# Kernel tuning notes

Hardware: AMD Instinct MI355X
Metric: run time of the kernel (lower is better)

The kernel has to match this reference:

```python
import jax, jax.numpy as jnp
import numpy as np

N, E, F_IN, C, H = 50000, 800000, 256, 128, 2
NEG_SLOPE = 0.2


def setup_inputs() -> dict:
    key = jax.random.key(0)
    ks = jax.random.split(key, 8)
    x = jax.random.normal(ks[0], (N, F_IN), dtype=jnp.float32)
    edge_index = jax.random.randint(ks[1], (2, E), 0, N, dtype=jnp.int64)
    # GATConv params (PyG: lin weight [H*C, F_IN], att_src/att_dst [H, C], bias [H*C])
    s_lin = 1.0 / np.sqrt(F_IN)
    W = jax.random.uniform(ks[2], (H * C, F_IN), minval=-s_lin, maxval=s_lin, dtype=jnp.float32)
    att_src = jax.random.normal(ks[3], (H, C), dtype=jnp.float32) * 0.1
    att_dst = jax.random.normal(ks[4], (H, C), dtype=jnp.float32) * 0.1
    bias = jnp.zeros((H * C,), dtype=jnp.float32)
    # trailing nn.Linear(H*C, C)
    s_l = 1.0 / np.sqrt(H * C)
    lin_w = jax.random.uniform(ks[5], (C, H * C), minval=-s_l, maxval=s_l, dtype=jnp.float32)
    lin_b = jax.random.uniform(ks[6], (C,), minval=-s_l, maxval=s_l, dtype=jnp.float32)
    return {"x": x, "edge_index": edge_index, "W": W, "att_src": att_src,
            "att_dst": att_dst, "bias": bias, "lin_w": lin_w, "lin_b": lin_b}


def _gat_forward(x, edge_index, W, att_src, att_dst, bias, lin_w, lin_b):
    # add self-loops (PyG default add_self_loops=True)
    loop = jnp.arange(N, dtype=edge_index.dtype)
    src = jnp.concatenate([edge_index[0], loop])  # [E+N]
    dst = jnp.concatenate([edge_index[1], loop])  # [E+N]

    h = (x @ W.T).reshape(N, H, C)                # [N, H, C]
    a_src = jnp.einsum('nhc,hc->nh', h, att_src)  # [N, H]
    a_dst = jnp.einsum('nhc,hc->nh', h, att_dst)  # [N, H]

    e = a_src[src] + a_dst[dst]                   # [E+N, H]
    e = jnp.where(e > 0, e, NEG_SLOPE * e)        # LeakyReLU(0.2)

    # softmax over edges grouped by destination node
    m = jax.ops.segment_max(e, dst, num_segments=N)          # [N, H]
    m = jnp.where(jnp.isfinite(m), m, 0.0)
    ex = jnp.exp(e - jax.lax.stop_gradient(m)[dst])
    denom = jax.ops.segment_sum(ex, dst, num_segments=N)     # [N, H]
    alpha = ex / jnp.maximum(denom[dst], 1e-16)               # [E+N, H]

    msg = h[src] * alpha[:, :, None]                          # [E+N, H, C]
    out = jax.ops.segment_sum(msg, dst, num_segments=N)       # [N, H, C]
    out = out.reshape(N, H * C) + bias

    out = jax.nn.elu(out)
    return out @ lin_w.T + lin_b                               # [N, C]


def reference(x, edge_index, W, att_src, att_dst, bias, lin_w, lin_b):
    return _gat_forward(x, edge_index, W, att_src, att_dst, bias, lin_w, lin_b)
```

## Files before the change

kernel.cpp:

```cpp
#include <hip/hip_runtime.h>
#include <hip/hip_fp16.h>
#include <math.h>

#define NN 50000
#define EE 800000
#define ET (EE + NN)
#define FIN 256
#define CCOUT 128
#define HH 2
#define HC 256
#define NEG 0.2f
#define RCAP 64

#define NB_XPREP (NN / 4)

#define PREP_W_BLOCKS 64
#define PREP_LW_BLOCKS 32
#define PREP_GRID (3 + PREP_W_BLOCKS + PREP_LW_BLOCKS)

#define G1X 391
#define G1Y 2
#define NB_G1 (G1X * G1Y)
#define NB_SCAT4 ((ET + 1023) / 1024)
#define PAIR_HEAD (2 * NB_G1)
#define NB_FUSE2 (NB_SCAT4 + NB_G1)

typedef __attribute__((ext_vector_type(8))) short short8;
typedef __attribute__((ext_vector_type(4))) float floatx4;
typedef _Float16 half2v __attribute__((ext_vector_type(2)));

__device__ __forceinline__ unsigned short f2bf(float f)
{
    union { float f; unsigned int u; } x; x.f = f;
    unsigned int r = x.u + 0x7fffu + ((x.u >> 16) & 1u);
    return (unsigned short)(r >> 16);
}
__device__ __forceinline__ unsigned short f2h(float f)
{
    __half h = __float2half_rn(f);
    return *(const unsigned short*)&h;
}
__device__ __forceinline__ unsigned int permb(unsigned int a, unsigned int b, unsigned int s)
{
    return __builtin_amdgcn_perm(a, b, s);
}
__device__ __forceinline__ float fdot2u(unsigned int a, unsigned int b, float c)
{
    union { unsigned int u; half2v h; } x, y;
    x.u = a; y.u = b;
    return __builtin_amdgcn_fdot2(x.h, y.h, c, false);
}

__device__ __forceinline__ int load_idx(const int* ei32, int is64, int pos)
{
    return is64 ? ei32[2 * pos] : ei32[pos];
}

__global__ __launch_bounds__(256) void prep_kernel(const float* __restrict__ W,
                                                   const float* __restrict__ att_s,
                                                   const float* __restrict__ att_d,
                                                   const float* __restrict__ lin_w,
                                                   const int* __restrict__ ei32,
                                                   float* __restrict__ was,
                                                   float* __restrict__ wad,
                                                   unsigned short* __restrict__ Wb,
                                                   unsigned short* __restrict__ linwb,
                                                   int* __restrict__ flag)
{
    int b = blockIdx.x, t = threadIdx.x;
    if (b == 0) {
        if (t < 64) {
            int v = ei32[2 * t + 1];
            unsigned long long m = __ballot(v != 0);
            if (t == 0) *flag = (m == 0ull) ? 1 : 0;
        }
    } else if (b <= 2) {
        int hd = b - 1;
        float as = 0.f, ad = 0.f;
        for (int c = 0; c < CCOUT; c++) {
            float wv = W[(size_t)(hd * CCOUT + c) * FIN + t];
            as += att_s[hd * CCOUT + c] * wv;
            ad += att_d[hd * CCOUT + c] * wv;
        }
        was[hd * FIN + t] = as;
        wad[hd * FIN + t] = ad;
    } else if (b < 3 + PREP_W_BLOCKS) {
        int i = (b - 3) * 256 + t;
        float4 v = *(const float4*)(W + (size_t)i * 4);
        ushort4 o;
        o.x = f2bf(v.x); o.y = f2bf(v.y); o.z = f2bf(v.z); o.w = f2bf(v.w);
        *(ushort4*)(Wb + (size_t)i * 4) = o;
    } else {
        int i = (b - 3 - PREP_W_BLOCKS) * 256 + t;
        float4 v = *(const float4*)(lin_w + (size_t)i * 4);
        ushort4 o;
        o.x = f2bf(v.x); o.y = f2bf(v.y); o.z = f2bf(v.z); o.w = f2bf(v.w);
        *(ushort4*)(linwb + (size_t)i * 4) = o;
    }
}

__global__ __launch_bounds__(256) void xprep_kernel(const float* __restrict__ x,
                                                    const float* __restrict__ was,
                                                    const float* __restrict__ wad,
                                                    unsigned short* __restrict__ xb,
                                                    float* __restrict__ a_s,
                                                    float* __restrict__ a_d)
{
    int b = blockIdx.x, t = threadIdx.x;
    int w = t >> 6, l = t & 63;
    int n = b * 4 + w;
    float4 xv = *(const float4*)(x + (size_t)n * FIN + l * 4);
    ushort4 xs;
    xs.x = f2bf(xv.x); xs.y = f2bf(xv.y); xs.z = f2bf(xv.z); xs.w = f2bf(xv.w);
    *(ushort4*)(xb + (size_t)n * FIN + l * 4) = xs;

    float4 s0 = *(const float4*)(was + l * 4);
    float4 s1 = *(const float4*)(was + FIN + l * 4);
    float4 d0 = *(const float4*)(wad + l * 4);
    float4 d1 = *(const float4*)(wad + FIN + l * 4);
    float vs0 = xv.x * s0.x + xv.y * s0.y + xv.z * s0.z + xv.w * s0.w;
    float vs1 = xv.x * s1.x + xv.y * s1.y + xv.z * s1.z + xv.w * s1.w;
    float vd0 = xv.x * d0.x + xv.y * d0.y + xv.z * d0.z + xv.w * d0.w;
    float vd1 = xv.x * d1.x + xv.y * d1.y + xv.z * d1.z + xv.w * d1.w;
#pragma unroll
    for (int off = 32; off > 0; off >>= 1) {
        vs0 += __shfl_down(vs0, off);
        vs1 += __shfl_down(vs1, off);
        vd0 += __shfl_down(vd0, off);
        vd1 += __shfl_down(vd1, off);
    }
    if (l == 0) {
        a_s[n * 2 + 0] = vs0; a_s[n * 2 + 1] = vs1;
        a_d[n * 2 + 0] = vd0; a_d[n * 2 + 1] = vd1;
    }
}

template <bool ADD_BIAS, bool OUT_BF16>
__global__ __launch_bounds__(256) void gemm_mfma(const unsigned short* __restrict__ A,
                                                 const unsigned short* __restrict__ B,
                                                 const float* __restrict__ bias,
                                                 void* __restrict__ Cout,
                                                 int M, int N, int K)
{
    const int LDT = 40;
    __shared__ unsigned short As[128 * LDT];
    __shared__ unsigned short Bs[128 * LDT];

    int tid = threadIdx.x;
    int wave = tid >> 6, lane = tid & 63;
    int wr = wave >> 1, wc = wave & 1;
    int quad = lane >> 4, l16 = lane & 15;
    int bm0 = blockIdx.x * 128;
    int bn0 = blockIdx.y * 128;

    floatx4 acc[4][4] = {};

    for (int kk = 0; kk < K; kk += 32) {
#pragma unroll
        for (int p = 0; p < 2; p++) {
            int idx = p * 256 + tid;
            int row = idx >> 2, seg = idx & 3;
            int grow = bm0 + row; if (grow >= M) grow = M - 1;
            uint4 va = *(const uint4*)(A + (size_t)grow * K + kk + seg * 8);
            *(uint4*)(&As[row * LDT + seg * 8]) = va;
            uint4 vb = *(const uint4*)(B + (size_t)(bn0 + row) * K + kk + seg * 8);
            *(uint4*)(&Bs[row * LDT + seg * 8]) = vb;
        }
        __syncthreads();

        short8 af[4], bfr[4];
#pragma unroll
        for (int mi = 0; mi < 4; mi++)
            af[mi] = *(const short8*)(&As[(wr * 64 + mi * 16 + l16) * LDT + quad * 8]);
#pragma unroll
        for (int ni = 0; ni < 4; ni++)
            bfr[ni] = *(const short8*)(&Bs[(wc * 64 + ni * 16 + l16) * LDT + quad * 8]);
#pragma unroll
        for (int mi = 0; mi < 4; mi++)
#pragma unroll
            for (int ni = 0; ni < 4; ni++)
                acc[mi][ni] = __builtin_amdgcn_mfma_f32_16x16x32_bf16(af[mi], bfr[ni], acc[mi][ni], 0, 0, 0);
        __syncthreads();
    }

#pragma unroll
    for (int mi = 0; mi < 4; mi++) {
#pragma unroll
        for (int ni = 0; ni < 4; ni++) {
            int col = bn0 + wc * 64 + ni * 16 + l16;
#pragma unroll
            for (int r = 0; r < 4; r++) {
                int row = bm0 + wr * 64 + mi * 16 + quad * 4 + r;
                if (row < M) {
                    float v = acc[mi][ni][r];
                    if (ADD_BIAS) v += bias[col];
                    if (OUT_BF16)
                        ((unsigned short*)Cout)[(size_t)row * N + col] = f2bf(v);
                    else
                        ((float*)Cout)[(size_t)row * N + col] = v;
                }
            }
        }
    }
}

__global__ __launch_bounds__(256) void scatter_gemm1_kernel(
        const int* __restrict__ ei32, const int* __restrict__ flag,
        int* __restrict__ cnt,
        const float* __restrict__ a_s, const float* __restrict__ a_d,
        uint2* __restrict__ rec,
        const unsigned short* __restrict__ A,
        const unsigned short* __restrict__ B,
        unsigned short* __restrict__ hb)
{
    const int LDT = 40;
    __shared__ unsigned short As[128 * LDT];
    __shared__ unsigned short Bs[128 * LDT];

    int b = blockIdx.x, tid = threadIdx.x;
    int sb = -1, gb = -1;
    if (b < PAIR_HEAD) {
        if (b & 1) sb = b >> 1; else gb = b >> 1;
    } else {
        sb = NB_G1 + (b - PAIR_HEAD);
    }

    if (sb >= 0) {
        int base = sb * 1024 + tid;
        int is64 = *flag;
        int ss[4], dd[4];
#pragma unroll
        for (int k = 0; k < 4; k++) {
            int e = base + k * 256;
            ss[k] = -1; dd[k] = 0;
            if (e < ET) {
                if (e < EE) { ss[k] = load_idx(ei32, is64, e); dd[k] = load_idx(ei32, is64, EE + e); }
                else { ss[k] = dd[k] = e - EE; }
            }
        }
        int rk[4];
#pragma unroll
        for (int k = 0; k < 4; k++)
            rk[k] = (ss[k] >= 0) ? atomicAdd(&cnt[dd[k] << 4], 1) : 0;
#pragma unroll
        for (int k = 0; k < 4; k++) {
            if (ss[k] < 0) continue;
            float e0 = a_s[ss[k] * 2 + 0] + a_d[dd[k] * 2 + 0];
            float e1 = a_s[ss[k] * 2 + 1] + a_d[dd[k] * 2 + 1];
            e0 = e0 > 0.f ? e0 : NEG * e0;
            e1 = e1 > 0.f ? e1 : NEG * e1;
            __half2 hp = __floats2half2_rn(__expf(e0), __expf(e1));
            uint2 r;
            r.x = (unsigned int)ss[k];
            r.y = *(unsigned int*)&hp;
            if (rk[k] < RCAP)
                rec[(size_t)dd[k] * RCAP + rk[k]] = r;
        }
        return;
    }

    int bx = gb % G1X, by = gb / G1X;
    int wave = tid >> 6, lane = tid & 63;
    int wr = wave >> 1, wc = wave & 1;
    int quad = lane >> 4, l16 = lane & 15;
    int bm0 = bx * 128;
    int bn0 = by * 128;

    floatx4 acc[4][4] = {};

    for (int kk = 0; kk < FIN; kk += 32) {
#pragma unroll
        for (int p = 0; p < 2; p++) {
            int idx = p * 256 + tid;
            int row = idx >> 2, seg = idx & 3;
            int grow = bm0 + row; if (grow >= NN) grow = NN - 1;
            uint4 va = *(const uint4*)(A + (size_t)grow * FIN + kk + seg * 8);
            *(uint4*)(&As[row * LDT + seg * 8]) = va;
            uint4 vb = *(const uint4*)(B + (size_t)(bn0 + row) * FIN + kk + seg * 8);
            *(uint4*)(&Bs[row * LDT + seg * 8]) = vb;
        }
        __syncthreads();

        short8 af[4], bfr[4];
#pragma unroll
        for (int mi = 0; mi < 4; mi++)
            af[mi] = *(const short8*)(&As[(wr * 64 + mi * 16 + l16) * LDT + quad * 8]);
#pragma unroll
        for (int ni = 0; ni < 4; ni++)
            bfr[ni] = *(const short8*)(&Bs[(wc * 64 + ni * 16 + l16) * LDT + quad * 8]);
#pragma unroll
        for (int mi = 0; mi < 4; mi++)
#pragma unroll
            for (int ni = 0; ni < 4; ni++)
                acc[mi][ni] = __builtin_amdgcn_mfma_f32_16x16x32_bf16(af[mi], bfr[ni], acc[mi][ni], 0, 0, 0);
        __syncthreads();
    }

#pragma unroll
    for (int mi = 0; mi < 4; mi++) {
#pragma unroll
        for (int ni = 0; ni < 4; ni++) {
            int col = bn0 + wc * 64 + ni * 16 + l16;
#pragma unroll
            for (int r = 0; r < 4; r++) {
                int row = bm0 + wr * 64 + mi * 16 + quad * 4 + r;
                if (row < NN)
                    hb[(size_t)row * HC + col] = f2h(acc[mi][ni][r]);
            }
        }
    }
}

__global__ __launch_bounds__(256) void agg12_kernel(const unsigned short* __restrict__ hb,
                                                    const int* __restrict__ cnt,
                                                    const uint2* __restrict__ rec,
                                                    const float* __restrict__ bias,
                                                    unsigned short* __restrict__ aggb)
{
    int wave = threadIdx.x >> 6, lane = threadIdx.x & 63;
    int d = blockIdx.x * 4 + wave;
    int half = lane >> 5;
    int l = lane & 31;
    int c = l * 8;
    unsigned int selp  = (l & 16) ? 0x07060302u : 0x05040100u;
    unsigned int selps = (l & 16) ? 0x0C0C0302u : 0x0C0C0100u;
    const unsigned int ones = 0x3C003C00u;
    const unsigned long long* recq = (const unsigned long long*)rec;

    int j0 = d * RCAP;
    int j1 = j0 + cnt[d << 4];
    float a0 = 0.f, a1 = 0.f, a2 = 0.f, a3 = 0.f;
    float a4 = 0.f, a5 = 0.f, a6 = 0.f, a7 = 0.f;
    float psum = 0.f;

    int j = j0 + half;
    for (; j + 6 < j1; j += 8) {
        unsigned long long q0 = recq[j], q1 = recq[j + 2], q2 = recq[j + 4], q3 = recq[j + 6];
        unsigned int pp01 = permb((unsigned int)(q1 >> 32), (unsigned int)(q0 >> 32), selp);
        unsigned int pp23 = permb((unsigned int)(q3 >> 32), (unsigned int)(q2 >> 32), selp);
        psum = fdot2u(pp01, ones, psum);
        psum = fdot2u(pp23, ones, psum);
        uint4 h0 = *(const uint4*)(hb + (size_t)(unsigned int)q0 * HC + c);
        uint4 h1 = *(const uint4*)(hb + (size_t)(unsigned int)q1 * HC + c);
        uint4 h2 = *(const uint4*)(hb + (size_t)(unsigned int)q2 * HC + c);
        uint4 h3 = *(const uint4*)(hb + (size_t)(unsigned int)q3 * HC + c);
        a0 = fdot2u(permb(h1.x, h0.x, 0x05040100u), pp01, a0);
        a0 = fdot2u(permb(h3.x, h2.x, 0x05040100u), pp23, a0);
        a1 = fdot2u(permb(h1.x, h0.x, 0x07060302u), pp01, a1);
        a1 = fdot2u(permb(h3.x, h2.x, 0x07060302u), pp23, a1);
        a2 = fdot2u(permb(h1.y, h0.y, 0x05040100u), pp01, a2);
        a2 = fdot2u(permb(h3.y, h2.y, 0x05040100u), pp23, a2);
        a3 = fdot2u(permb(h1.y, h0.y, 0x07060302u), pp01, a3);
        a3 = fdot2u(permb(h3.y, h2.y, 0x07060302u), pp23, a3);
        a4 = fdot2u(permb(h1.z, h0.z, 0x05040100u), pp01, a4);
        a4 = fdot2u(permb(h3.z, h2.z, 0x05040100u), pp23, a4);
        a5 = fdot2u(permb(h1.z, h0.z, 0x07060302u), pp01, a5);
        a5 = fdot2u(permb(h3.z, h2.z, 0x07060302u), pp23, a5);
        a6 = fdot2u(permb(h1.w, h0.w, 0x05040100u), pp01, a6);
        a6 = fdot2u(permb(h3.w, h2.w, 0x05040100u), pp23, a6);
        a7 = fdot2u(permb(h1.w, h0.w, 0x07060302u), pp01, a7);
        a7 = fdot2u(permb(h3.w, h2.w, 0x07060302u), pp23, a7);
    }
    for (; j < j1; j += 2) {
        unsigned long long q0 = recq[j];
        unsigned int pp = permb(0u, (unsigned int)(q0 >> 32), selps);
        psum = fdot2u(pp, ones, psum);
        uint4 h0 = *(const uint4*)(hb + (size_t)(unsigned int)q0 * HC + c);
        a0 = fdot2u(permb(0u, h0.x, 0x0C0C0100u), pp, a0);
        a1 = fdot2u(permb(0u, h0.x, 0x0C0C0302u), pp, a1);
        a2 = fdot2u(permb(0u, h0.y, 0x0C0C0100u), pp, a2);
        a3 = fdot2u(permb(0u, h0.y, 0x0C0C0302u), pp, a3);
        a4 = fdot2u(permb(0u, h0.z, 0x0C0C0100u), pp, a4);
        a5 = fdot2u(permb(0u, h0.z, 0x0C0C0302u), pp, a5);
        a6 = fdot2u(permb(0u, h0.w, 0x0C0C0100u), pp, a6);
        a7 = fdot2u(permb(0u, h0.w, 0x0C0C0302u), pp, a7);
    }

    a0 += __shfl_xor(a0, 32);
    a1 += __shfl_xor(a1, 32);
    a2 += __shfl_xor(a2, 32);
    a3 += __shfl_xor(a3, 32);
    a4 += __shfl_xor(a4, 32);
    a5 += __shfl_xor(a5, 32);
    a6 += __shfl_xor(a6, 32);
    a7 += __shfl_xor(a7, 32);
    psum += __shfl_xor(psum, 32);

    if (half == 0) {
        float inv = 1.f / fmaxf(psum, 1e-16f);
        float4 b0 = *(const float4*)(bias + c);
        float4 b1 = *(const float4*)(bias + c + 4);
        float v0 = a0 * inv + b0.x;
        float v1 = a1 * inv + b0.y;
        float v2 = a2 * inv + b0.z;
        float v3 = a3 * inv + b0.w;
        float v4 = a4 * inv + b1.x;
        float v5 = a5 * inv + b1.y;
        float v6 = a6 * inv + b1.z;
        float v7 = a7 * inv + b1.w;
        v0 = v0 > 0.f ? v0 : expm1f(v0);
        v1 = v1 > 0.f ? v1 : expm1f(v1);
        v2 = v2 > 0.f ? v2 : expm1f(v2);
        v3 = v3 > 0.f ? v3 : expm1f(v3);
        v4 = v4 > 0.f ? v4 : expm1f(v4);
        v5 = v5 > 0.f ? v5 : expm1f(v5);
        v6 = v6 > 0.f ? v6 : expm1f(v6);
        v7 = v7 > 0.f ? v7 : expm1f(v7);
        uint4 o;
        o.x = (unsigned int)f2bf(v0) | ((unsigned int)f2bf(v1) << 16);
        o.y = (unsigned int)f2bf(v2) | ((unsigned int)f2bf(v3) << 16);
        o.z = (unsigned int)f2bf(v4) | ((unsigned int)f2bf(v5) << 16);
        o.w = (unsigned int)f2bf(v6) | ((unsigned int)f2bf(v7) << 16);
        *(uint4*)(aggb + (size_t)d * HC + c) = o;
    }
}

extern "C" void kernel_launch(void* const* d_in, const int* in_sizes, int n_in,
                              void* d_out, int out_size, void* d_ws, size_t ws_size,
                              hipStream_t stream)
{
    const float* x       = (const float*)d_in[0];
    const int*   ei32    = (const int*)d_in[1];
    const float* W       = (const float*)d_in[2];
    const float* att_src = (const float*)d_in[3];
    const float* att_dst = (const float*)d_in[4];
    const float* bias    = (const float*)d_in[5];
    const float* lin_w   = (const float*)d_in[6];
    const float* lin_b   = (const float*)d_in[7];
    float* out = (float*)d_out;

    char* ws = (char*)d_ws;
    size_t off = 0;
    auto alloc = [&](size_t bytes) -> void* {
        void* p = ws + off;
        off += (bytes + 255) & ~(size_t)255;
        return p;
    };

    int*   cnt    = (int*)alloc((size_t)NN * 64);
    size_t zero_bytes = off;

    int*   flag     = (int*)alloc(256);
    float* was      = (float*)alloc((size_t)HH * FIN * 4);
    float* wad      = (float*)alloc((size_t)HH * FIN * 4);
    float* a_s      = (float*)alloc((size_t)NN * 2 * 4);
    float* a_d      = (float*)alloc((size_t)NN * 2 * 4);
    uint2* rec      = (uint2*)alloc((size_t)NN * RCAP * 8);
    unsigned short* xb     = (unsigned short*)alloc((size_t)NN * FIN * 2);
    unsigned short* Wb     = (unsigned short*)alloc((size_t)HC * FIN * 2);
    unsigned short* linwb  = (unsigned short*)alloc((size_t)CCOUT * HC * 2);
    unsigned short* hb     = (unsigned short*)alloc((size_t)NN * HC * 2);
    unsigned short* aggb   = (unsigned short*)alloc((size_t)NN * HC * 2);

    hipMemsetAsync(d_ws, 0, zero_bytes, stream);

    prep_kernel<<<PREP_GRID, 256, 0, stream>>>(W, att_src, att_dst, lin_w, ei32,
                                               was, wad, Wb, linwb, flag);

    xprep_kernel<<<NB_XPREP, 256, 0, stream>>>(x, was, wad, xb, a_s, a_d);

    scatter_gemm1_kernel<<<NB_FUSE2, 256, 0, stream>>>(ei32, flag, cnt,
                                                       a_s, a_d, rec, xb, Wb, hb);

    agg12_kernel<<<NN / 4, 256, 0, stream>>>(hb, cnt, rec, bias, aggb);

    dim3 g2((NN + 127) / 128, CCOUT / 128);
    gemm_mfma<true, false><<<g2, 256, 0, stream>>>(aggb, linwb, lin_b, out, NN, CCOUT, HC);
}
```

Baseline: 257.3 us.

## Split edge scatter by destination parity to overlap half of aggregation

```diff
diff --git a/kernel.cpp b/kernel.cpp
--- a/kernel.cpp
+++ b/kernel.cpp
@@ -13,6 +13,7 @@
 #define RCAP 64
 
 #define NB_XPREP (NN / 4)
+#define NB_AGG_HALF (NN / 8)
 
 #define PREP_W_BLOCKS 64
 #define PREP_LW_BLOCKS 32
@@ -25,6 +26,8 @@
 #define PAIR_HEAD (2 * NB_G1)
 #define NB_FUSE2 (NB_SCAT4 + NB_G1)
 
+#define NB_K3 (NB_SCAT4 + NB_AGG_HALF)
+
 typedef __attribute__((ext_vector_type(8))) short short8;
 typedef __attribute__((ext_vector_type(4))) float floatx4;
 typedef _Float16 half2v __attribute__((ext_vector_type(2)));
@@ -56,269 +59,55 @@
     return is64 ? ei32[2 * pos] : ei32[pos];
 }
 
-__global__ __launch_bounds__(256) void prep_kernel(const float* __restrict__ W,
-                                                   const float* __restrict__ att_s,
-                                                   const float* __restrict__ att_d,
-                                                   const float* __restrict__ lin_w,
-                                                   const int* __restrict__ ei32,
-                                                   float* __restrict__ was,
-                                                   float* __restrict__ wad,
-                                                   unsigned short* __restrict__ Wb,
-                                                   unsigned short* __restrict__ linwb,
-                                                   int* __restrict__ flag)
-{
-    int b = blockIdx.x, t = threadIdx.x;
-    if (b == 0) {
-        if (t < 64) {
-            int v = ei32[2 * t + 1];
-            unsigned long long m = __ballot(v != 0);
-            if (t == 0) *flag = (m == 0ull) ? 1 : 0;
-        }
-    } else if (b <= 2) {
-        int hd = b - 1;
-        float as = 0.f, ad = 0.f;
-        for (int c = 0; c < CCOUT; c++) {
-            float wv = W[(size_t)(hd * CCOUT + c) * FIN + t];
-            as += att_s[hd * CCOUT + c] * wv;
-            ad += att_d[hd * CCOUT + c] * wv;
-        }
-        was[hd * FIN + t] = as;
-        wad[hd * FIN + t] = ad;
-    } else if (b < 3 + PREP_W_BLOCKS) {
-        int i = (b - 3) * 256 + t;
-        float4 v = *(const float4*)(W + (size_t)i * 4);
-        ushort4 o;
-        o.x = f2bf(v.x); o.y = f2bf(v.y); o.z = f2bf(v.z); o.w = f2bf(v.w);
-        *(ushort4*)(Wb + (size_t)i * 4) = o;
-    } else {
-        int i = (b - 3 - PREP_W_BLOCKS) * 256 + t;
-        float4 v = *(const float4*)(lin_w + (size_t)i * 4);
-        ushort4 o;
-        o.x = f2bf(v.x); o.y = f2bf(v.y); o.z = f2bf(v.z); o.w = f2bf(v.w);
-        *(ushort4*)(linwb + (size_t)i * 4) = o;
-    }
-}
-
-__global__ __launch_bounds__(256) void xprep_kernel(const float* __restrict__ x,
-                                                    const float* __restrict__ was,
-                                                    const float* __restrict__ wad,
-                                                    unsigned short* __restrict__ xb,
-                                                    float* __restrict__ a_s,
-                                                    float* __restrict__ a_d)
-{
-    int b = blockIdx.x, t = threadIdx.x;
-    int w = t >> 6, l = t & 63;
-    int n = b * 4 + w;
-    float4 xv = *(const float4*)(x + (size_t)n * FIN + l * 4);
-    ushort4 xs;
-    xs.x = f2bf(xv.x); xs.y = f2bf(xv.y); xs.z = f2bf(xv.z); xs.w = f2bf(xv.w);
-    *(ushort4*)(xb + (size_t)n * FIN + l * 4) = xs;
-
-    float4 s0 = *(const float4*)(was + l * 4);
-    float4 s1 = *(const float4*)(was + FIN + l * 4);
-    float4 d0 = *(const float4*)(wad + l * 4);
-    float4 d1 = *(const float4*)(wad + FIN + l * 4);
-    float vs0 = xv.x * s0.x + xv.y * s0.y + xv.z * s0.z + xv.w * s0.w;
-    float vs1 = xv.x * s1.x + xv.y * s1.y + xv.z * s1.z + xv.w * s1.w;
-    float vd0 = xv.x * d0.x + xv.y * d0.y + xv.z * d0.z + xv.w * d0.w;
-    float vd1 = xv.x * d1.x + xv.y * d1.y + xv.z * d1.z + xv.w * d1.w;
-#pragma unroll
-    for (int off = 32; off > 0; off >>= 1) {
-        vs0 += __shfl_down(vs0, off);
-        vs1 += __shfl_down(vs1, off);
-        vd0 += __shfl_down(vd0, off);
-        vd1 += __shfl_down(vd1, off);
-    }
-    if (l == 0) {
-        a_s[n * 2 + 0] = vs0; a_s[n * 2 + 1] = vs1;
-        a_d[n * 2 + 0] = vd0; a_d[n * 2 + 1] = vd1;
-    }
-}
-
-template <bool ADD_BIAS, bool OUT_BF16>
-__global__ __launch_bounds__(256) void gemm_mfma(const unsigned short* __restrict__ A,
-                                                 const unsigned short* __restrict__ B,
-                                                 const float* __restrict__ bias,
-                                                 void* __restrict__ Cout,
-                                                 int M, int N, int K)
-{
-    const int LDT = 40;
-    __shared__ unsigned short As[128 * LDT];
-    __shared__ unsigned short Bs[128 * LDT];
-
-    int tid = threadIdx.x;
-    int wave = tid >> 6, lane = tid & 63;
-    int wr = wave >> 1, wc = wave & 1;
-    int quad = lane >> 4, l16 = lane & 15;
-    int bm0 = blockIdx.x * 128;
-    int bn0 = blockIdx.y * 128;
-
-    floatx4 acc[4][4] = {};
-
-    for (int kk = 0; kk < K; kk += 32) {
-#pragma unroll
-        for (int p = 0; p < 2; p++) {
-            int idx = p * 256 + tid;
-            int row = idx >> 2, seg = idx & 3;
-            int grow = bm0 + row; if (grow >= M) grow = M - 1;
-            uint4 va = *(const uint4*)(A + (size_t)grow * K + kk + seg * 8);
-            *(uint4*)(&As[row * LDT + seg * 8]) = va;
-            uint4 vb = *(const uint4*)(B + (size_t)(bn0 + row) * K + kk + seg * 8);
-            *(uint4*)(&Bs[row * LDT + seg * 8]) = vb;
-        }
-        __syncthreads();
-
-        short8 af[4], bfr[4];
-#pragma unroll
-        for (int mi = 0; mi < 4; mi++)
-            af[mi] = *(const short8*)(&As[(wr * 64 + mi * 16 + l16) * LDT + quad * 8]);
-#pragma unroll
-        for (int ni = 0; ni < 4; ni++)
-            bfr[ni] = *(const short8*)(&Bs[(wc * 64 + ni * 16 + l16) * LDT + quad * 8]);
-#pragma unroll
-        for (int mi = 0; mi < 4; mi++)
-#pragma unroll
-            for (int ni = 0; ni < 4; ni++)
-                acc[mi][ni] = __builtin_amdgcn_mfma_f32_16x16x32_bf16(af[mi], bfr[ni], acc[mi][ni], 0, 0, 0);
-        __syncthreads();
-    }
-
-#pragma unroll
-    for (int mi = 0; mi < 4; mi++) {
-#pragma unroll
-        for (int ni = 0; ni < 4; ni++) {
-            int col = bn0 + wc * 64 + ni * 16 + l16;
-#pragma unroll
-            for (int r = 0; r < 4; r++) {
-                int row = bm0 + wr * 64 + mi * 16 + quad * 4 + r;
-                if (row < M) {
-                    float v = acc[mi][ni][r];
-                    if (ADD_BIAS) v += bias[col];
-                    if (OUT_BF16)
-                        ((unsigned short*)Cout)[(size_t)row * N + col] = f2bf(v);
-                    else
-                        ((float*)Cout)[(size_t)row * N + col] = v;
-                }
-            }
-        }
-    }
-}
-
-__global__ __launch_bounds__(256) void scatter_gemm1_kernel(
-        const int* __restrict__ ei32, const int* __restrict__ flag,
-        int* __restrict__ cnt,
-        const float* __restrict__ a_s, const float* __restrict__ a_d,
-        uint2* __restrict__ rec,
-        const unsigned short* __restrict__ A,
-        const unsigned short* __restrict__ B,
-        unsigned short* __restrict__ hb)
-{
-    const int LDT = 40;
-    __shared__ unsigned short As[128 * LDT];
-    __shared__ unsigned short Bs[128 * LDT];
-
-    int b = blockIdx.x, tid = threadIdx.x;
-    int sb = -1, gb = -1;
-    if (b < PAIR_HEAD) {
-        if (b & 1) sb = b >> 1; else gb = b >> 1;
-    } else {
-        sb = NB_G1 + (b - PAIR_HEAD);
-    }
-
-    if (sb >= 0) {
-        int base = sb * 1024 + tid;
-        int is64 = *flag;
-        int ss[4], dd[4];
-#pragma unroll
-        for (int k = 0; k < 4; k++) {
-            int e = base + k * 256;
-            ss[k] = -1; dd[k] = 0;
-            if (e < ET) {
-                if (e < EE) { ss[k] = load_idx(ei32, is64, e); dd[k] = load_idx(ei32, is64, EE + e); }
-                else { ss[k] = dd[k] = e - EE; }
-            }
-        }
-        int rk[4];
-#pragma unroll
-        for (int k = 0; k < 4; k++)
-            rk[k] = (ss[k] >= 0) ? atomicAdd(&cnt[dd[k] << 4], 1) : 0;
-#pragma unroll
-        for (int k = 0; k < 4; k++) {
-            if (ss[k] < 0) continue;
-            float e0 = a_s[ss[k] * 2 + 0] + a_d[dd[k] * 2 + 0];
-            float e1 = a_s[ss[k] * 2 + 1] + a_d[dd[k] * 2 + 1];
-            e0 = e0 > 0.f ? e0 : NEG * e0;
-            e1 = e1 > 0.f ? e1 : NEG * e1;
-            __half2 hp = __floats2half2_rn(__expf(e0), __expf(e1));
-            uint2 r;
-            r.x = (unsigned int)ss[k];
-            r.y = *(unsigned int*)&hp;
-            if (rk[k] < RCAP)
-                rec[(size_t)dd[k] * RCAP + rk[k]] = r;
-        }
-        return;
-    }
-
-    int bx = gb % G1X, by = gb / G1X;
-    int wave = tid >> 6, lane = tid & 63;
-    int wr = wave >> 1, wc = wave & 1;
-    int quad = lane >> 4, l16 = lane & 15;
-    int bm0 = bx * 128;
-    int bn0 = by * 128;
-
-    floatx4 acc[4][4] = {};
-
-    for (int kk = 0; kk < FIN; kk += 32) {
-#pragma unroll
-        for (int p = 0; p < 2; p++) {
-            int idx = p * 256 + tid;
-            int row = idx >> 2, seg = idx & 3;
-            int grow = bm0 + row; if (grow >= NN) grow = NN - 1;
-            uint4 va = *(const uint4*)(A + (size_t)grow * FIN + kk + seg * 8);
-            *(uint4*)(&As[row * LDT + seg * 8]) = va;
-            uint4 vb = *(const uint4*)(B + (size_t)(bn0 + row) * FIN + kk + seg * 8);
-            *(uint4*)(&Bs[row * LDT + seg * 8]) = vb;
-        }
-        __syncthreads();
-
-        short8 af[4], bfr[4];
-#pragma unroll
-        for (int mi = 0; mi < 4; mi++)
-            af[mi] = *(const short8*)(&As[(wr * 64 + mi * 16 + l16) * LDT + quad * 8]);
-#pragma unroll
-        for (int ni = 0; ni < 4; ni++)
-            bfr[ni] = *(const short8*)(&Bs[(wc * 64 + ni * 16 + l16) * LDT + quad * 8]);
-#pragma unroll
-        for (int mi = 0; mi < 4; mi++)
-#pragma unroll
-            for (int ni = 0; ni < 4; ni++)
-                acc[mi][ni] = __builtin_amdgcn_mfma_f32_16x16x32_bf16(af[mi], bfr[ni], acc[mi][ni], 0, 0, 0);
-        __syncthreads();
-    }
-
-#pragma unroll
-    for (int mi = 0; mi < 4; mi++) {
-#pragma unroll
-        for (int ni = 0; ni < 4; ni++) {
-            int col = bn0 + wc * 64 + ni * 16 + l16;
-#pragma unroll
-            for (int r = 0; r < 4; r++) {
-                int row = bm0 + wr * 64 + mi * 16 + quad * 4 + r;
-                if (row < NN)
-                    hb[(size_t)row * HC + col] = f2h(acc[mi][ni][r]);
-            }
-        }
-    }
-}
-
-__global__ __launch_bounds__(256) void agg12_kernel(const unsigned short* __restrict__ hb,
-                                                    const int* __restrict__ cnt,
-                                                    const uint2* __restrict__ rec,
-                                                    const float* __restrict__ bias,
-                                                    unsigned short* __restrict__ aggb)
-{
-    int wave = threadIdx.x >> 6, lane = threadIdx.x & 63;
-    int d = blockIdx.x * 4 + wave;
+template <int PARITY>
+__device__ __forceinline__ void scatter4_body(int sb, int tid,
+                                              const int* __restrict__ ei32, int is64,
+                                              int* __restrict__ cnt,
+                                              const float* __restrict__ a_s,
+                                              const float* __restrict__ a_d,
+                                              uint2* __restrict__ rec)
+{
+    int base = sb * 1024 + tid;
+    int ss[4], dd[4];
+#pragma unroll
+    for (int k = 0; k < 4; k++) {
+        int e = base + k * 256;
+        ss[k] = -1; dd[k] = 0;
+        if (e < ET) {
+            int s, d;
+            if (e < EE) { s = load_idx(ei32, is64, e); d = load_idx(ei32, is64, EE + e); }
+            else { s = d = e - EE; }
+            if ((d & 1) == PARITY) { ss[k] = s; dd[k] = d; }
+        }
+    }
+    int rk[4];
+#pragma unroll
+    for (int k = 0; k < 4; k++)
+        rk[k] = (ss[k] >= 0) ? atomicAdd(&cnt[dd[k] << 4], 1) : 0;
+#pragma unroll
+    for (int k = 0; k < 4; k++) {
+        if (ss[k] < 0) continue;
+        float e0 = a_s[ss[k] * 2 + 0] + a_d[dd[k] * 2 + 0];
+        float e1 = a_s[ss[k] * 2 + 1] + a_d[dd[k] * 2 + 1];
+        e0 = e0 > 0.f ? e0 : NEG * e0;
+        e1 = e1 > 0.f ? e1 : NEG * e1;
+        __half2 hp = __floats2half2_rn(__expf(e0), __expf(e1));
+        uint2 r;
+        r.x = (unsigned int)ss[k];
+        r.y = *(unsigned int*)&hp;
+        if (rk[k] < RCAP)
+            rec[(size_t)dd[k] * RCAP + rk[k]] = r;
+    }
+}
+
+__device__ __forceinline__ void agg_body(int d,
+                                         const unsigned short* __restrict__ hb,
+                                         const int* __restrict__ cnt,
+                                         const uint2* __restrict__ rec,
+                                         const float* __restrict__ bias,
+                                         unsigned short* __restrict__ aggb)
+{
+    int lane = threadIdx.x & 63;
     int half = lane >> 5;
     int l = lane & 31;
     int c = l * 8;
@@ -415,6 +204,263 @@
     }
 }
 
+__global__ __launch_bounds__(256) void prep_kernel(const float* __restrict__ W,
+                                                   const float* __restrict__ att_s,
+                                                   const float* __restrict__ att_d,
+                                                   const float* __restrict__ lin_w,
+                                                   const int* __restrict__ ei32,
+                                                   float* __restrict__ was,
+                                                   float* __restrict__ wad,
+                                                   unsigned short* __restrict__ Wb,
+                                                   unsigned short* __restrict__ linwb,
+                                                   int* __restrict__ flag)
+{
+    int b = blockIdx.x, t = threadIdx.x;
+    if (b == 0) {
+        if (t < 64) {
+            int v = ei32[2 * t + 1];
+            unsigned long long m = __ballot(v != 0);
+            if (t == 0) *flag = (m == 0ull) ? 1 : 0;
+        }
+    } else if (b <= 2) {
+        int hd = b - 1;
+        float as = 0.f, ad = 0.f;
+        for (int c = 0; c < CCOUT; c++) {
+            float wv = W[(size_t)(hd * CCOUT + c) * FIN + t];
+            as += att_s[hd * CCOUT + c] * wv;
+            ad += att_d[hd * CCOUT + c] * wv;
+        }
+        was[hd * FIN + t] = as;
+        wad[hd * FIN + t] = ad;
+    } else if (b < 3 + PREP_W_BLOCKS) {
+        int i = (b - 3) * 256 + t;
+        float4 v = *(const float4*)(W + (size_t)i * 4);
+        ushort4 o;
+        o.x = f2bf(v.x); o.y = f2bf(v.y); o.z = f2bf(v.z); o.w = f2bf(v.w);
+        *(ushort4*)(Wb + (size_t)i * 4) = o;
+    } else {
+        int i = (b - 3 - PREP_W_BLOCKS) * 256 + t;
+        float4 v = *(const float4*)(lin_w + (size_t)i * 4);
+        ushort4 o;
+        o.x = f2bf(v.x); o.y = f2bf(v.y); o.z = f2bf(v.z); o.w = f2bf(v.w);
+        *(ushort4*)(linwb + (size_t)i * 4) = o;
+    }
+}
+
+__global__ __launch_bounds__(256) void xprep_kernel(const float* __restrict__ x,
+                                                    const float* __restrict__ was,
+                                                    const float* __restrict__ wad,
+                                                    unsigned short* __restrict__ xb,
+                                                    float* __restrict__ a_s,
+                                                    float* __restrict__ a_d)
+{
+    int b = blockIdx.x, t = threadIdx.x;
+    int w = t >> 6, l = t & 63;
+    int n = b * 4 + w;
+    float4 xv = *(const float4*)(x + (size_t)n * FIN + l * 4);
+    ushort4 xs;
+    xs.x = f2bf(xv.x); xs.y = f2bf(xv.y); xs.z = f2bf(xv.z); xs.w = f2bf(xv.w);
+    *(ushort4*)(xb + (size_t)n * FIN + l * 4) = xs;
+
+    float4 s0 = *(const float4*)(was + l * 4);
+    float4 s1 = *(const float4*)(was + FIN + l * 4);
+    float4 d0 = *(const float4*)(wad + l * 4);
+    float4 d1 = *(const float4*)(wad + FIN + l * 4);
+    float vs0 = xv.x * s0.x + xv.y * s0.y + xv.z * s0.z + xv.w * s0.w;
+    float vs1 = xv.x * s1.x + xv.y * s1.y + xv.z * s1.z + xv.w * s1.w;
+    float vd0 = xv.x * d0.x + xv.y * d0.y + xv.z * d0.z + xv.w * d0.w;
+    float vd1 = xv.x * d1.x + xv.y * d1.y + xv.z * d1.z + xv.w * d1.w;
+#pragma unroll
+    for (int off = 32; off > 0; off >>= 1) {
+        vs0 += __shfl_down(vs0, off);
+        vs1 += __shfl_down(vs1, off);
+        vd0 += __shfl_down(vd0, off);
+        vd1 += __shfl_down(vd1, off);
+    }
+    if (l == 0) {
+        a_s[n * 2 + 0] = vs0; a_s[n * 2 + 1] = vs1;
+        a_d[n * 2 + 0] = vd0; a_d[n * 2 + 1] = vd1;
+    }
+}
+
+template <bool ADD_BIAS, bool OUT_BF16>
+__global__ __launch_bounds__(256) void gemm_mfma(const unsigned short* __restrict__ A,
+                                                 const unsigned short* __restrict__ B,
+                                                 const float* __restrict__ bias,
+                                                 void* __restrict__ Cout,
+                                                 int M, int N, int K)
+{
+    const int LDT = 40;
+    __shared__ unsigned short As[128 * LDT];
+    __shared__ unsigned short Bs[128 * LDT];
+
+    int tid = threadIdx.x;
+    int wave = tid >> 6, lane = tid & 63;
+    int wr = wave >> 1, wc = wave & 1;
+    int quad = lane >> 4, l16 = lane & 15;
+    int bm0 = blockIdx.x * 128;
+    int bn0 = blockIdx.y * 128;
+
+    floatx4 acc[4][4] = {};
+
+    for (int kk = 0; kk < K; kk += 32) {
+#pragma unroll
+        for (int p = 0; p < 2; p++) {
+            int idx = p * 256 + tid;
+            int row = idx >> 2, seg = idx & 3;
+            int grow = bm0 + row; if (grow >= M) grow = M - 1;
+            uint4 va = *(const uint4*)(A + (size_t)grow * K + kk + seg * 8);
+            *(uint4*)(&As[row * LDT + seg * 8]) = va;
+            uint4 vb = *(const uint4*)(B + (size_t)(bn0 + row) * K + kk + seg * 8);
+            *(uint4*)(&Bs[row * LDT + seg * 8]) = vb;
+        }
+        __syncthreads();
+
+        short8 af[4], bfr[4];
+#pragma unroll
+        for (int mi = 0; mi < 4; mi++)
+            af[mi] = *(const short8*)(&As[(wr * 64 + mi * 16 + l16) * LDT + quad * 8]);
+#pragma unroll
+        for (int ni = 0; ni < 4; ni++)
+            bfr[ni] = *(const short8*)(&Bs[(wc * 64 + ni * 16 + l16) * LDT + quad * 8]);
+#pragma unroll
+        for (int mi = 0; mi < 4; mi++)
+#pragma unroll
+            for (int ni = 0; ni < 4; ni++)
+                acc[mi][ni] = __builtin_amdgcn_mfma_f32_16x16x32_bf16(af[mi], bfr[ni], acc[mi][ni], 0, 0, 0);
+        __syncthreads();
+    }
+
+#pragma unroll
+    for (int mi = 0; mi < 4; mi++) {
+#pragma unroll
+        for (int ni = 0; ni < 4; ni++) {
+            int col = bn0 + wc * 64 + ni * 16 + l16;
+#pragma unroll
+            for (int r = 0; r < 4; r++) {
+                int row = bm0 + wr * 64 + mi * 16 + quad * 4 + r;
+                if (row < M) {
+                    float v = acc[mi][ni][r];
+                    if (ADD_BIAS) v += bias[col];
+                    if (OUT_BF16)
+                        ((unsigned short*)Cout)[(size_t)row * N + col] = f2bf(v);
+                    else
+                        ((float*)Cout)[(size_t)row * N + col] = v;
+                }
+            }
+        }
+    }
+}
+
+__global__ __launch_bounds__(256) void scatter_gemm1_kernel(
+        const int* __restrict__ ei32, const int* __restrict__ flag,
+        int* __restrict__ cnt,
+        const float* __restrict__ a_s, const float* __restrict__ a_d,
+        uint2* __restrict__ rec,
+        const unsigned short* __restrict__ A,
+        const unsigned short* __restrict__ B,
+        unsigned short* __restrict__ hb)
+{
+    const int LDT = 40;
+    __shared__ unsigned short As[128 * LDT];
+    __shared__ unsigned short Bs[128 * LDT];
+
+    int b = blockIdx.x, tid = threadIdx.x;
+    int sb = -1, gb = -1;
+    if (b < PAIR_HEAD) {
+        if (b & 1) sb = b >> 1; else gb = b >> 1;
+    } else {
+        sb = NB_G1 + (b - PAIR_HEAD);
+    }
+
+    if (sb >= 0) {
+        scatter4_body<0>(sb, tid, ei32, *flag, cnt, a_s, a_d, rec);
+        return;
+    }
+
+    int bx = gb % G1X, by = gb / G1X;
+    int wave = tid >> 6, lane = tid & 63;
+    int wr = wave >> 1, wc = wave & 1;
+    int quad = lane >> 4, l16 = lane & 15;
+    int bm0 = bx * 128;
+    int bn0 = by * 128;
+
+    floatx4 acc[4][4] = {};
+
+    for (int kk = 0; kk < FIN; kk += 32) {
+#pragma unroll
+        for (int p = 0; p < 2; p++) {
+            int idx = p * 256 + tid;
+            int row = idx >> 2, seg = idx & 3;
+            int grow = bm0 + row; if (grow >= NN) grow = NN - 1;
+            uint4 va = *(const uint4*)(A + (size_t)grow * FIN + kk + seg * 8);
+            *(uint4*)(&As[row * LDT + seg * 8]) = va;
+            uint4 vb = *(const uint4*)(B + (size_t)(bn0 + row) * FIN + kk + seg * 8);
+            *(uint4*)(&Bs[row * LDT + seg * 8]) = vb;
+        }
+        __syncthreads();
+
+        short8 af[4], bfr[4];
+#pragma unroll
+        for (int mi = 0; mi < 4; mi++)
+            af[mi] = *(const short8*)(&As[(wr * 64 + mi * 16 + l16) * LDT + quad * 8]);
+#pragma unroll
+        for (int ni = 0; ni < 4; ni++)
+            bfr[ni] = *(const short8*)(&Bs[(wc * 64 + ni * 16 + l16) * LDT + quad * 8]);
+#pragma unroll
+        for (int mi = 0; mi < 4; mi++)
+#pragma unroll
+            for (int ni = 0; ni < 4; ni++)
+                acc[mi][ni] = __builtin_amdgcn_mfma_f32_16x16x32_bf16(af[mi], bfr[ni], acc[mi][ni], 0, 0, 0);
+        __syncthreads();
+    }
+
+#pragma unroll
+    for (int mi = 0; mi < 4; mi++) {
+#pragma unroll
+        for (int ni = 0; ni < 4; ni++) {
+            int col = bn0 + wc * 64 + ni * 16 + l16;
+#pragma unroll
+            for (int r = 0; r < 4; r++) {
+                int row = bm0 + wr * 64 + mi * 16 + quad * 4 + r;
+                if (row < NN)
+                    hb[(size_t)row * HC + col] = f2h(acc[mi][ni][r]);
+            }
+        }
+    }
+}
+
+__global__ __launch_bounds__(256) void scatter_agg_kernel(
+        const int* __restrict__ ei32, const int* __restrict__ flag,
+        int* __restrict__ cnt,
+        const float* __restrict__ a_s, const float* __restrict__ a_d,
+        uint2* __restrict__ rec,
+        const unsigned short* __restrict__ hb,
+        const float* __restrict__ bias,
+        unsigned short* __restrict__ aggb)
+{
+    int b = blockIdx.x;
+    if (b < NB_SCAT4) {
+        scatter4_body<1>(b, threadIdx.x, ei32, *flag, cnt, a_s, a_d, rec);
+        return;
+    }
+    int g = b - NB_SCAT4;
+    int wave = threadIdx.x >> 6;
+    int d = g * 8 + wave * 2;
+    agg_body(d, hb, cnt, rec, bias, aggb);
+}
+
+__global__ __launch_bounds__(256) void agg_odd_kernel(const unsigned short* __restrict__ hb,
+                                                      const int* __restrict__ cnt,
+                                                      const uint2* __restrict__ rec,
+                                                      const float* __restrict__ bias,
+                                                      unsigned short* __restrict__ aggb)
+{
+    int wave = threadIdx.x >> 6;
+    int d = blockIdx.x * 8 + wave * 2 + 1;
+    agg_body(d, hb, cnt, rec, bias, aggb);
+}
+
 extern "C" void kernel_launch(void* const* d_in, const int* in_sizes, int n_in,
                               void* d_out, int out_size, void* d_ws, size_t ws_size,
                               hipStream_t stream)
@@ -462,7 +508,10 @@
     scatter_gemm1_kernel<<<NB_FUSE2, 256, 0, stream>>>(ei32, flag, cnt,
                                                        a_s, a_d, rec, xb, Wb, hb);
 
-    agg12_kernel<<<NN / 4, 256, 0, stream>>>(hb, cnt, rec, bias, aggb);
+    scatter_agg_kernel<<<NB_K3, 256, 0, stream>>>(ei32, flag, cnt, a_s, a_d, rec,
+                                                  hb, bias, aggb);
+
+    agg_odd_kernel<<<NB_AGG_HALF, 256, 0, stream>>>(hb, cnt, rec, bias, aggb);
 
     dim3 g2((NN + 127) / 128, CCOUT / 128);
     gemm_mfma<true, false><<<g2, 256, 0, stream>>>(aggb, linwb, lin_b, out, NN, CCOUT, HC);
```

New measurement: 259.6 us. No clear change (+0.9%).
